# Kernel tuning notes

Hardware: AMD Instinct MI355X
Metric: run time of the kernel (lower is better)

Reference implementation:

```python
import jax, jax.numpy as jnp
import numpy as np

B = 128
N = 65536          # total nodes across batched subgraphs
E = 1048576        # total edges
CLIP_DIM = 768
PD = 512           # projection_dim


def setup_inputs() -> dict:
    key = jax.random.key(0)
    ks = jax.random.split(key, 20)
    s = 0.02
    return {
        # CLIP-encoded features (clip encoders treated as upstream feature extractors)
        "image_features": jax.random.normal(ks[0], (B, CLIP_DIM), jnp.float32),
        "text_features": jax.random.normal(ks[1], (B, CLIP_DIM), jnp.float32),
        "answer": jax.random.uniform(ks[2], (B,), jnp.float32),
        # batched subgraph (X_fixed rows already gathered, as in extract_subgraph_batch)
        "x_nodes": jax.random.normal(ks[3], (N, PD), jnp.float32),
        "edge_index": jax.random.randint(ks[4], (2, E), 0, N, jnp.int32),
        "batch_vec": jnp.sort(jax.random.randint(ks[5], (N,), 0, B, jnp.int32)),
        # image/text projections (clip_dim != projection_dim -> Linear)
        "W_img": jax.random.normal(ks[6], (CLIP_DIM, PD), jnp.float32) * s,
        "b_img": jnp.zeros((PD,), jnp.float32),
        "W_txt": jax.random.normal(ks[7], (CLIP_DIM, PD), jnp.float32) * s,
        "b_txt": jnp.zeros((PD,), jnp.float32),
        # implicit classifier: Linear(2*PD, PD) -> ReLU -> Linear(PD, 1)
        "W1": jax.random.normal(ks[8], (2 * PD, PD), jnp.float32) * s,
        "b1": jnp.zeros((PD,), jnp.float32),
        "W2": jax.random.normal(ks[9], (PD, 1), jnp.float32) * s,
        "b2": jnp.zeros((1,), jnp.float32),
        # GCNConv(PD, PD)
        "Wg": jax.random.normal(ks[10], (PD, PD), jnp.float32) * s,
        "bg": jnp.zeros((PD,), jnp.float32),
        # symbolic classifier: Linear(PD, PD) -> ReLU -> Linear(PD, 1)
        "Ws1": jax.random.normal(ks[11], (PD, PD), jnp.float32) * s,
        "bs1": jnp.zeros((PD,), jnp.float32),
        "Ws2": jax.random.normal(ks[12], (PD, 1), jnp.float32) * s,
        "bs2": jnp.zeros((1,), jnp.float32),
    }


def gcn_conv(x, edge_index, W, b):
    """PyG GCNConv: h = W x; add self-loops; sym-normalized sum aggregation."""
    n = x.shape[0]
    h = x @ W                                     # [N, PD] dense GEMM
    loop = jnp.arange(n, dtype=edge_index.dtype)
    src = jnp.concatenate([edge_index[0], loop])  # [E+N]
    dst = jnp.concatenate([edge_index[1], loop])
    deg = jax.ops.segment_sum(jnp.ones_like(dst, dtype=h.dtype), dst, num_segments=n)
    dis = jax.lax.rsqrt(deg)                      # deg >= 1 (self loops)
    norm = dis[src] * dis[dst]                    # [E+N]
    out = jax.ops.segment_sum(h[src] * norm[:, None], dst, num_segments=n)
    return out + b


def reference(image_features, text_features, answer, x_nodes, edge_index, batch_vec,
              W_img, b_img, W_txt, b_txt, W1, b1, W2, b2,
              Wg, bg, Ws1, bs1, Ws2, bs2):
    # ---- implicit branch (MedicalVQAModel.forward) ----
    img = image_features @ W_img + b_img          # [B, PD]
    txt = text_features @ W_txt + b_txt           # [B, PD]
    combined = jnp.concatenate([img, txt], axis=-1)
    h = jax.nn.relu(combined @ W1 + b1)           # dropout p=0.1 inactive (eval)
    y_implicit = (h @ W2 + b2)[:, 0]              # [B]

    # ---- symbolic branch: GCN over batched subgraphs ----
    x = gcn_conv(x_nodes, edge_index, Wg, bg)
    x = jax.nn.relu(x)                            # dropout p=0.8 inactive (eval)
    bv = batch_vec.astype(jnp.int32)
    sums = jax.ops.segment_sum(x, bv, num_segments=B)          # [B, PD]
    cnts = jax.ops.segment_sum(jnp.ones((x.shape[0],), x.dtype), bv, num_segments=B)
    graph_features = sums / jnp.maximum(cnts, 1.0)[:, None]    # global_mean_pool
    hs = jax.nn.relu(graph_features @ Ws1 + bs1)
    y_symbolic = (hs @ Ws2 + bs2)[:, 0]           # [B]

    logits = jnp.maximum(y_implicit, y_symbolic)
    # BCEWithLogits (mean): log(1+e^l) - l*y
    loss = jnp.mean(jnp.logaddexp(0.0, logits) - logits * answer)
    return (logits, loss)
```

## Files before the change

### kernel.cpp

```cpp
#include <hip/hip_runtime.h>
#include <stdint.h>

#define N_NODES 65536
#define N_EDGES 1048576
#define BATCH   128
#define PD      512
#define CLIPD   768

typedef __attribute__((ext_vector_type(4))) float f32x4;
typedef __attribute__((ext_vector_type(2))) float f32x2;
typedef __attribute__((ext_vector_type(4))) int   i32x4;

__device__ __forceinline__ unsigned short f2b(float f) {
    uint32_t u = __float_as_uint(f);
    return (unsigned short)((u + 0x7fffu + ((u >> 16) & 1u)) >> 16);
}

__global__ void k_wgt(const float* __restrict__ Wg, unsigned short* __restrict__ WgT,
                      const int* __restrict__ bv, int* __restrict__ cnts) {
    __shared__ float tile[32][33];
    int kb = blockIdx.x * 32, nb = blockIdx.y * 32;
    int tx = threadIdx.x, ty = threadIdx.y;
    if (kb == 0 && nb == 0) {
        int tid = ty * 32 + tx;
        if (tid < BATCH) {
            int lo = 0, hi = N_NODES;
            while (lo < hi) { int m = (lo + hi) >> 1; if (bv[m] < tid) lo = m + 1; else hi = m; }
            int lo2 = lo, hi2 = N_NODES;
            while (lo2 < hi2) { int m = (lo2 + hi2) >> 1; if (bv[m] < tid + 1) lo2 = m + 1; else hi2 = m; }
            cnts[tid] = lo2 - lo;
        }
    }
    tile[ty][tx] = Wg[(size_t)(kb + ty) * PD + nb + tx];
    __syncthreads();
    WgT[(size_t)(nb + ty) * PD + kb + tx] = f2b(tile[tx][ty]);
}

__global__ void k_init(int* __restrict__ deg, int* __restrict__ fill,
                       float* __restrict__ sums) {
    int i = blockIdx.x * 256 + threadIdx.x;
    deg[i] = 1;
    fill[i] = 0;
    sums[i] = 0.f;
}

__global__ void k_deg(const int* __restrict__ ei, int* __restrict__ deg) {
    int e = blockIdx.x * 256 + threadIdx.x;
    atomicAdd(&deg[ei[N_EDGES + e]], 1);
}

__global__ void k_scan(const int* __restrict__ deg, int* __restrict__ row_ptr,
                       float* __restrict__ dis) {
    __shared__ int wsum[16];
    const int t = threadIdx.x;
    const int w = t >> 6, l = t & 63;
    const int base = w * 4096;
    int s = 0;
    for (int i = 0; i < 64; ++i) s += deg[base + i * 64 + l];
    s -= 64;
#pragma unroll
    for (int off = 1; off < 64; off <<= 1) s += __shfl_xor(s, off);
    if (l == 0) wsum[w] = s;
    __syncthreads();
    int carry = 0;
    for (int i = 0; i < 16; ++i) carry += (i < w) ? wsum[i] : 0;
    int idx = base + l;
    int d = deg[idx];
    for (int i = 0; i < 64; ++i) {
        int dn = 0;
        if (i < 63) dn = deg[idx + 64];
        int v = d - 1;
        int inc = v;
#pragma unroll
        for (int off = 1; off < 64; off <<= 1) {
            int n = __shfl_up(inc, off);
            if (l >= off) inc += n;
        }
        row_ptr[idx] = carry + inc - v;
        dis[idx] = rsqrtf((float)d);
        carry += __shfl(inc, 63);
        idx += 64;
        d = dn;
    }
    if (t == 1023) row_ptr[N_NODES] = carry;
}

__global__ void k_scatter(const int* __restrict__ ei, const int* __restrict__ row_ptr,
                          int* __restrict__ fill, int* __restrict__ srcs) {
    int e = blockIdx.x * 256 + threadIdx.x;
    int d = ei[N_EDGES + e];
    int pos = row_ptr[d] + atomicAdd(&fill[d], 1);
    srcs[pos] = ei[e];
}

__device__ __forceinline__ void mfma16(f32x4& acc, i32x4 a, i32x4 b) {
    asm("v_mfma_f32_16x16x32_bf16 %0, %1, %2, %0" : "+v"(acc) : "v"(a), "v"(b));
}

__global__ __launch_bounds__(256) void k_gemm(const float* __restrict__ X,
                                              const unsigned short* __restrict__ WgT,
                                              const float* __restrict__ dis,
                                              uint8_t* __restrict__ hn8) {
    __shared__ __align__(16) unsigned short As[128 * 32];
    __shared__ __align__(16) unsigned short Bs[256 * 32];
    const int m0 = blockIdx.x * 128;
    const int n0 = blockIdx.y * 256;
    const int t = threadIdx.x;
    const int lane = t & 63, w = t >> 6;
    const int wr = w >> 1, wc = w & 1;
    const int g = lane >> 4, lr = lane & 15;

    f32x4 acc[4][8] = {};

    for (int k0 = 0; k0 < PD; k0 += 32) {
        __syncthreads();
#pragma unroll
        for (int it = 0; it < 4; ++it) {
            int idx = it * 256 + t;
            int r = idx >> 3, kc = (idx & 7) * 4;
            float4 v = *(const float4*)&X[(size_t)(m0 + r) * PD + k0 + kc];
            uint2 o;
            o.x = (uint32_t)f2b(v.x) | ((uint32_t)f2b(v.y) << 16);
            o.y = (uint32_t)f2b(v.z) | ((uint32_t)f2b(v.w) << 16);
            *(uint2*)&As[r * 32 + kc] = o;
        }
#pragma unroll
        for (int it = 0; it < 4; ++it) {
            int idx = it * 256 + t;
            int r = idx >> 2, kc = (idx & 3) * 8;
            *(uint4*)&Bs[r * 32 + kc] = *(const uint4*)&WgT[(size_t)(n0 + r) * PD + k0 + kc];
        }
        __syncthreads();

        i32x4 a[4], b[8];
#pragma unroll
        for (int i = 0; i < 4; ++i) a[i] = *(const i32x4*)&As[(wr * 64 + i * 16 + lr) * 32 + g * 8];
#pragma unroll
        for (int j = 0; j < 8; ++j) b[j] = *(const i32x4*)&Bs[(wc * 128 + j * 16 + lr) * 32 + g * 8];
#pragma unroll
        for (int i = 0; i < 4; ++i)
#pragma unroll
            for (int j = 0; j < 8; ++j) mfma16(acc[i][j], a[i], b[j]);
    }
    asm volatile("s_nop 7\n s_nop 7\n s_nop 7\n s_nop 7");

#pragma unroll
    for (int i = 0; i < 4; ++i) {
#pragma unroll
        for (int r = 0; r < 4; ++r) {
            int row = m0 + wr * 64 + i * 16 + g * 4 + r;
            float dd = dis[row];
#pragma unroll
            for (int j = 0; j < 8; ++j) {
                int col = n0 + wc * 128 + j * 16 + lr;
                float val = acc[i][j][r] * dd;
                uint32_t p = __builtin_amdgcn_cvt_pk_fp8_f32(val, val, 0, false);
                hn8[(size_t)row * PD + col] = (uint8_t)p;
            }
        }
    }
}

#define NPB 8
__global__ __launch_bounds__(256) void k_agg(const uint8_t* __restrict__ hn8,
                                             const float* __restrict__ dis,
                                             const float* __restrict__ bg,
                                             const int* __restrict__ row_ptr,
                                             const int* __restrict__ srcs,
                                             const int* __restrict__ bv,
                                             float* __restrict__ sums) {
    __shared__ __align__(16) float cmb[128 * 4];
    const int t = threadIdx.x;
    const int half = t >> 7, tl = t & 127;
    const int c0 = tl * 4;
    const int node0 = blockIdx.x * NPB;
    const float bg0 = bg[c0], bg1 = bg[c0 + 1], bg2 = bg[c0 + 2], bg3 = bg[c0 + 3];
    float s0 = 0.f, s1 = 0.f, s2 = 0.f, s3 = 0.f;
    int curb = bv[node0];
    for (int ni = 0; ni < NPB; ++ni) {
        int node = node0 + ni;
        int b = bv[node];
        if (b != curb) {
            if (half == 0) {
                atomicAdd(&sums[(size_t)curb * PD + c0 + 0], s0);
                atomicAdd(&sums[(size_t)curb * PD + c0 + 1], s1);
                atomicAdd(&sums[(size_t)curb * PD + c0 + 2], s2);
                atomicAdd(&sums[(size_t)curb * PD + c0 + 3], s3);
            }
            s0 = s1 = s2 = s3 = 0.f;
            curb = b;
        }
        float a0 = 0.f, a1 = 0.f, a2 = 0.f, a3 = 0.f;
        int beg = row_ptr[node], end = row_ptr[node + 1];
        int e = beg + half;
        for (; e + 14 < end; e += 16) {
            int sn[8];
#pragma unroll
            for (int q = 0; q < 8; ++q) sn[q] = srcs[e + 2 * q];
            uint32_t v[8];
#pragma unroll
            for (int q = 0; q < 8; ++q)
                v[q] = *(const uint32_t*)&hn8[(size_t)sn[q] * PD + c0];
#pragma unroll
            for (int q = 0; q < 8; ++q) {
                f32x2 lo = __builtin_amdgcn_cvt_pk_f32_fp8(v[q], false);
                f32x2 hi = __builtin_amdgcn_cvt_pk_f32_fp8(v[q], true);
                a0 += lo[0]; a1 += lo[1]; a2 += hi[0]; a3 += hi[1];
            }
        }
        for (; e < end; e += 2) {
            uint32_t v = *(const uint32_t*)&hn8[(size_t)srcs[e] * PD + c0];
            f32x2 lo = __builtin_amdgcn_cvt_pk_f32_fp8(v, false);
            f32x2 hi = __builtin_amdgcn_cvt_pk_f32_fp8(v, true);
            a0 += lo[0]; a1 += lo[1]; a2 += hi[0]; a3 += hi[1];
        }
        if (half == 1) {
            uint32_t v = *(const uint32_t*)&hn8[(size_t)node * PD + c0];
            f32x2 lo = __builtin_amdgcn_cvt_pk_f32_fp8(v, false);
            f32x2 hi = __builtin_amdgcn_cvt_pk_f32_fp8(v, true);
            a0 += lo[0]; a1 += lo[1]; a2 += hi[0]; a3 += hi[1];
            f32x4 wv = {a0, a1, a2, a3};
            *(f32x4*)&cmb[tl * 4] = wv;
        }
        __syncthreads();
        if (half == 0) {
            f32x4 ov = *(const f32x4*)&cmb[tl * 4];
            float dd = dis[node];
            a0 = fmaxf(fmaf(a0 + ov[0], dd, bg0), 0.f);
            a1 = fmaxf(fmaf(a1 + ov[1], dd, bg1), 0.f);
            a2 = fmaxf(fmaf(a2 + ov[2], dd, bg2), 0.f);
            a3 = fmaxf(fmaf(a3 + ov[3], dd, bg3), 0.f);
            s0 += a0; s1 += a1; s2 += a2; s3 += a3;
        }
        __syncthreads();
    }
    if (half == 0) {
        atomicAdd(&sums[(size_t)curb * PD + c0 + 0], s0);
        atomicAdd(&sums[(size_t)curb * PD + c0 + 1], s1);
        atomicAdd(&sums[(size_t)curb * PD + c0 + 2], s2);
        atomicAdd(&sums[(size_t)curb * PD + c0 + 3], s3);
    }
}

__device__ __forceinline__ void lin_part_core(const float* __restrict__ a,
                                              const float* __restrict__ wp,
                                              float* __restrict__ P, int slot, int c0) {
    float acc0 = 0.f, acc1 = 0.f, acc2 = 0.f, acc3 = 0.f;
    float acc4 = 0.f, acc5 = 0.f, acc6 = 0.f, acc7 = 0.f;
#pragma unroll 4
    for (int k = 0; k < 256; k += 8) {
        float a0 = a[k + 0], a1 = a[k + 1], a2 = a[k + 2], a3 = a[k + 3];
        float a4 = a[k + 4], a5 = a[k + 5], a6 = a[k + 6], a7 = a[k + 7];
        float2 w0 = *(const float2*)&wp[(size_t)(k + 0) * PD];
        float2 w1 = *(const float2*)&wp[(size_t)(k + 1) * PD];
        float2 w2 = *(const float2*)&wp[(size_t)(k + 2) * PD];
        float2 w3 = *(const float2*)&wp[(size_t)(k + 3) * PD];
        float2 w4 = *(const float2*)&wp[(size_t)(k + 4) * PD];
        float2 w5 = *(const float2*)&wp[(size_t)(k + 5) * PD];
        float2 w6 = *(const float2*)&wp[(size_t)(k + 6) * PD];
        float2 w7 = *(const float2*)&wp[(size_t)(k + 7) * PD];
        acc0 = fmaf(a0, w0.x, acc0); acc1 = fmaf(a0, w0.y, acc1);
        acc2 = fmaf(a1, w1.x, acc2); acc3 = fmaf(a1, w1.y, acc3);
        acc4 = fmaf(a2, w2.x, acc4); acc5 = fmaf(a2, w2.y, acc5);
        acc6 = fmaf(a3, w3.x, acc6); acc7 = fmaf(a3, w3.y, acc7);
        acc0 = fmaf(a4, w4.x, acc0); acc1 = fmaf(a4, w4.y, acc1);
        acc2 = fmaf(a5, w5.x, acc2); acc3 = fmaf(a5, w5.y, acc3);
        acc4 = fmaf(a6, w6.x, acc4); acc5 = fmaf(a6, w6.y, acc5);
        acc6 = fmaf(a7, w7.x, acc6); acc7 = fmaf(a7, w7.y, acc7);
    }
    P[(size_t)slot * PD + c0] = (acc0 + acc2) + (acc4 + acc6);
    P[(size_t)slot * PD + c0 + 1] = (acc1 + acc3) + (acc5 + acc7);
}

__global__ __launch_bounds__(256) void k_lin_part(const float* __restrict__ A,
                                                  const float* __restrict__ W,
                                                  float* __restrict__ P, int K) {
    const int row = blockIdx.x, kc = blockIdx.y, c0 = threadIdx.x * 2;
    lin_part_core(A + (size_t)row * K + kc * 256, W + (size_t)kc * 256 * PD + c0,
                  P, row * 8 + kc, c0);
}

__global__ __launch_bounds__(256) void k_lin_part_it(const float* __restrict__ IMG,
                                                     const float* __restrict__ TXT,
                                                     const float* __restrict__ Wi,
                                                     const float* __restrict__ Wt,
                                                     float* __restrict__ P) {
    const int row = blockIdx.x, kc = blockIdx.y, c0 = threadIdx.x * 2;
    const float* A = (kc < 3) ? IMG : TXT;
    const float* W = (kc < 3) ? Wi : Wt;
    const int sub = (kc < 3) ? kc : kc - 3;
    lin_part_core(A + (size_t)row * CLIPD + sub * 256, W + (size_t)sub * 256 * PD + c0,
                  P, row * 8 + kc, c0);
}

__global__ __launch_bounds__(256) void k_lin_red_it(const float* __restrict__ P,
                                                    const float* __restrict__ bi,
                                                    const float* __restrict__ bt,
                                                    float* __restrict__ C) {
    const int row = blockIdx.x, side = blockIdx.y, c0 = threadIdx.x * 2;
    const float* p = P + ((size_t)row * 8 + side * 3) * PD + c0;
    float r0 = p[0] + p[PD] + p[2 * PD];
    float r1 = p[1] + p[PD + 1] + p[2 * PD + 1];
    const float* bias = side ? bt : bi;
    C[(size_t)row * 1024 + side * PD + c0] = r0 + bias[c0];
    C[(size_t)row * 1024 + side * PD + c0 + 1] = r1 + bias[c0 + 1];
}

__global__ __launch_bounds__(256) void k_reddot(const float* __restrict__ P,
                                                const float* __restrict__ bias,
                                                const float* __restrict__ w2,
                                                const float* __restrict__ b2,
                                                float* __restrict__ y,
                                                int nch, const int* __restrict__ cnts) {
    __shared__ float wred[4];
    const int row = blockIdx.x;
    const int t = threadIdx.x;
    const int c0 = t * 2;
    const float* p = P + (size_t)row * 8 * PD + c0;
    float r0 = p[0], r1 = p[1];
    if (nch > 1) { r0 += p[PD];     r1 += p[PD + 1]; }
    if (nch > 2) { r0 += p[2 * PD]; r1 += p[2 * PD + 1]; }
    if (nch > 3) { r0 += p[3 * PD]; r1 += p[3 * PD + 1]; }
    float s = 1.f;
    if (cnts) s = 1.f / fmaxf((float)cnts[row], 1.f);
    r0 = fmaxf(fmaf(r0, s, bias[c0]), 0.f);
    r1 = fmaxf(fmaf(r1, s, bias[c0 + 1]), 0.f);
    float partial = fmaf(r0, w2[c0], r1 * w2[c0 + 1]);
#pragma unroll
    for (int off = 32; off; off >>= 1) partial += __shfl_down(partial, off);
    if ((t & 63) == 0) wred[t >> 6] = partial;
    __syncthreads();
    if (t == 0) y[row] = (wred[0] + wred[1]) + (wred[2] + wred[3]) + b2[0];
}

__global__ void k_final(const float* __restrict__ yi, const float* __restrict__ ys,
                        const float* __restrict__ ans, float* __restrict__ out) {
    __shared__ float red[128];
    int t = threadIdx.x;
    float l = fmaxf(yi[t], ys[t]);
    out[t] = l;
    float li = fmaxf(l, 0.f) + log1pf(expf(-fabsf(l))) - l * ans[t];
    red[t] = li;
    __syncthreads();
    for (int off = 64; off; off >>= 1) {
        if (t < off) red[t] += red[t + off];
        __syncthreads();
    }
    if (t == 0) out[BATCH] = red[0] / (float)BATCH;
}

extern "C" void kernel_launch(void* const* d_in, const int* in_sizes, int n_in,
                              void* d_out, int out_size, void* d_ws, size_t ws_size,
                              hipStream_t stream) {
    const float* image_features = (const float*)d_in[0];
    const float* text_features  = (const float*)d_in[1];
    const float* answer         = (const float*)d_in[2];
    const float* x_nodes        = (const float*)d_in[3];
    const int*   edge_index     = (const int*)d_in[4];
    const int*   batch_vec      = (const int*)d_in[5];
    const float* W_img = (const float*)d_in[6];
    const float* b_img = (const float*)d_in[7];
    const float* W_txt = (const float*)d_in[8];
    const float* b_txt = (const float*)d_in[9];
    const float* W1  = (const float*)d_in[10];
    const float* b1  = (const float*)d_in[11];
    const float* W2  = (const float*)d_in[12];
    const float* b2  = (const float*)d_in[13];
    const float* Wg  = (const float*)d_in[14];
    const float* bg  = (const float*)d_in[15];
    const float* Ws1 = (const float*)d_in[16];
    const float* bs1 = (const float*)d_in[17];
    const float* Ws2 = (const float*)d_in[18];
    const float* bs2 = (const float*)d_in[19];
    float* out = (float*)d_out;

    char* base = (char*)d_ws;
    size_t cur = 0;
    auto alloc = [&](size_t bytes) -> void* {
        void* r = base + cur;
        cur = (cur + bytes + 255) & ~(size_t)255;
        return r;
    };
    unsigned short* WgT = (unsigned short*)alloc((size_t)PD * PD * 2);
    uint8_t* hn8   = (uint8_t*)alloc((size_t)N_NODES * PD);
    int*   deg     = (int*)alloc((size_t)N_NODES * 4);
    float* dis     = (float*)alloc((size_t)N_NODES * 4);
    int*   row_ptr = (int*)alloc((size_t)(N_NODES + 1) * 4);
    int*   fill    = (int*)alloc((size_t)N_NODES * 4);
    int*   srcs    = (int*)alloc((size_t)N_EDGES * 4);
    float* sums    = (float*)alloc((size_t)BATCH * PD * 4);
    int*   cnts    = (int*)alloc((size_t)BATCH * 4);
    float* Ppart   = (float*)alloc((size_t)BATCH * 8 * PD * 4);
    float* combined = (float*)alloc((size_t)BATCH * 1024 * 4);
    float* yi      = (float*)alloc((size_t)BATCH * 4);
    float* ys      = (float*)alloc((size_t)BATCH * 4);

    hipLaunchKernelGGL(k_wgt, dim3(16, 16), dim3(32, 32), 0, stream, Wg, WgT, batch_vec, cnts);
    hipLaunchKernelGGL(k_init, dim3(256), dim3(256), 0, stream, deg, fill, sums);
    hipLaunchKernelGGL(k_deg, dim3(4096), dim3(256), 0, stream, edge_index, deg);
    hipLaunchKernelGGL(k_scan, dim3(1), dim3(1024), 0, stream, deg, row_ptr, dis);
    hipLaunchKernelGGL(k_scatter, dim3(4096), dim3(256), 0, stream, edge_index, row_ptr, fill, srcs);
    hipLaunchKernelGGL(k_gemm, dim3(N_NODES / 128, PD / 256), dim3(256), 0, stream,
                       x_nodes, WgT, dis, hn8);
    hipLaunchKernelGGL(k_agg, dim3(N_NODES / NPB), dim3(256), 0, stream,
                       hn8, dis, bg, row_ptr, srcs, batch_vec, sums);

    hipLaunchKernelGGL(k_lin_part_it, dim3(BATCH, 6), dim3(256), 0, stream,
                       image_features, text_features, W_img, W_txt, Ppart);
    hipLaunchKernelGGL(k_lin_red_it, dim3(BATCH, 2), dim3(256), 0, stream,
                       Ppart, b_img, b_txt, combined);
    hipLaunchKernelGGL(k_lin_part, dim3(BATCH, 4), dim3(256), 0, stream,
                       combined, W1, Ppart, 1024);
    hipLaunchKernelGGL(k_reddot, dim3(BATCH), dim3(256), 0, stream,
                       Ppart, b1, W2, b2, yi, 4, (const int*)nullptr);

    hipLaunchKernelGGL(k_lin_part, dim3(BATCH, 2), dim3(256), 0, stream,
                       sums, Ws1, Ppart, PD);
    hipLaunchKernelGGL(k_reddot, dim3(BATCH), dim3(256), 0, stream,
                       Ppart, bs1, Ws2, bs2, ys, 2, cnts);

    hipLaunchKernelGGL(k_final, dim3(1), dim3(128), 0, stream, yi, ys, answer, out);
}
```

Baseline: 411.8 us.

## Assign one wavefront per node run in GCN aggregation, drop block syncs

The aggregation kernel changes from a 256-thread block splitting each node's edges across two halves, which were combined through shared memory with two __syncthreads per node, to each 64-lane wavefront handling its own run of 8 nodes. Each lane now covers 8 channels with 8-byte fp8 loads. This removes the shared-memory combine and block barriers and widens per-lane gathers. In exchange each node's edges are walked serially by one wave, so per-node latency grows, and there are four times as many atomic streams into the pooled sums.

```diff
diff --git a/kernel.cpp b/kernel.cpp
--- a/kernel.cpp
+++ b/kernel.cpp
@@ -161,7 +161,16 @@
     }
 }
 
-#define NPB 8
+#define NPW 8
+__device__ __forceinline__ void acc8(float a[8], uint2 v) {
+    f32x2 l0 = __builtin_amdgcn_cvt_pk_f32_fp8(v.x, false);
+    f32x2 h0 = __builtin_amdgcn_cvt_pk_f32_fp8(v.x, true);
+    f32x2 l1 = __builtin_amdgcn_cvt_pk_f32_fp8(v.y, false);
+    f32x2 h1 = __builtin_amdgcn_cvt_pk_f32_fp8(v.y, true);
+    a[0] += l0[0]; a[1] += l0[1]; a[2] += h0[0]; a[3] += h0[1];
+    a[4] += l1[0]; a[5] += l1[1]; a[6] += h1[0]; a[7] += h1[1];
+}
+
 __global__ __launch_bounds__(256) void k_agg(const uint8_t* __restrict__ hn8,
                                              const float* __restrict__ dis,
                                              const float* __restrict__ bg,
@@ -169,77 +178,56 @@
                                              const int* __restrict__ srcs,
                                              const int* __restrict__ bv,
                                              float* __restrict__ sums) {
-    __shared__ __align__(16) float cmb[128 * 4];
     const int t = threadIdx.x;
-    const int half = t >> 7, tl = t & 127;
-    const int c0 = tl * 4;
-    const int node0 = blockIdx.x * NPB;
-    const float bg0 = bg[c0], bg1 = bg[c0 + 1], bg2 = bg[c0 + 2], bg3 = bg[c0 + 3];
-    float s0 = 0.f, s1 = 0.f, s2 = 0.f, s3 = 0.f;
+    const int w = t >> 6, lane = t & 63;
+    const int c0 = lane * 8;
+    const int node0 = (blockIdx.x * 4 + w) * NPW;
+    float bgv[8];
+#pragma unroll
+    for (int j = 0; j < 8; ++j) bgv[j] = bg[c0 + j];
+    float s[8] = {};
     int curb = bv[node0];
-    for (int ni = 0; ni < NPB; ++ni) {
+    for (int ni = 0; ni < NPW; ++ni) {
         int node = node0 + ni;
         int b = bv[node];
         if (b != curb) {
-            if (half == 0) {
-                atomicAdd(&sums[(size_t)curb * PD + c0 + 0], s0);
-                atomicAdd(&sums[(size_t)curb * PD + c0 + 1], s1);
-                atomicAdd(&sums[(size_t)curb * PD + c0 + 2], s2);
-                atomicAdd(&sums[(size_t)curb * PD + c0 + 3], s3);
-            }
-            s0 = s1 = s2 = s3 = 0.f;
+#pragma unroll
+            for (int j = 0; j < 8; ++j) atomicAdd(&sums[(size_t)curb * PD + c0 + j], s[j]);
+#pragma unroll
+            for (int j = 0; j < 8; ++j) s[j] = 0.f;
             curb = b;
         }
-        float a0 = 0.f, a1 = 0.f, a2 = 0.f, a3 = 0.f;
+        float a[8] = {};
         int beg = row_ptr[node], end = row_ptr[node + 1];
-        int e = beg + half;
-        for (; e + 14 < end; e += 16) {
+        int e = beg;
+        for (; e + 8 <= end; e += 8) {
             int sn[8];
 #pragma unroll
-            for (int q = 0; q < 8; ++q) sn[q] = srcs[e + 2 * q];
-            uint32_t v[8];
+            for (int q = 0; q < 8; ++q) sn[q] = srcs[e + q];
+            uint2 v[8];
 #pragma unroll
             for (int q = 0; q < 8; ++q)
-                v[q] = *(const uint32_t*)&hn8[(size_t)sn[q] * PD + c0];
-#pragma unroll
-            for (int q = 0; q < 8; ++q) {
-                f32x2 lo = __builtin_amdgcn_cvt_pk_f32_fp8(v[q], false);
-                f32x2 hi = __builtin_amdgcn_cvt_pk_f32_fp8(v[q], true);
-                a0 += lo[0]; a1 += lo[1]; a2 += hi[0]; a3 += hi[1];
-            }
-        }
-        for (; e < end; e += 2) {
-            uint32_t v = *(const uint32_t*)&hn8[(size_t)srcs[e] * PD + c0];
-            f32x2 lo = __builtin_amdgcn_cvt_pk_f32_fp8(v, false);
-            f32x2 hi = __builtin_amdgcn_cvt_pk_f32_fp8(v, true);
-            a0 += lo[0]; a1 += lo[1]; a2 += hi[0]; a3 += hi[1];
-        }
-        if (half == 1) {
-            uint32_t v = *(const uint32_t*)&hn8[(size_t)node * PD + c0];
-            f32x2 lo = __builtin_amdgcn_cvt_pk_f32_fp8(v, false);
-            f32x2 hi = __builtin_amdgcn_cvt_pk_f32_fp8(v, true);
-            a0 += lo[0]; a1 += lo[1]; a2 += hi[0]; a3 += hi[1];
-            f32x4 wv = {a0, a1, a2, a3};
-            *(f32x4*)&cmb[tl * 4] = wv;
-        }
-        __syncthreads();
-        if (half == 0) {
-            f32x4 ov = *(const f32x4*)&cmb[tl * 4];
-            float dd = dis[node];
-            a0 = fmaxf(fmaf(a0 + ov[0], dd, bg0), 0.f);
-            a1 = fmaxf(fmaf(a1 + ov[1], dd, bg1), 0.f);
-            a2 = fmaxf(fmaf(a2 + ov[2], dd, bg2), 0.f);
-            a3 = fmaxf(fmaf(a3 + ov[3], dd, bg3), 0.f);
-            s0 += a0; s1 += a1; s2 += a2; s3 += a3;
-        }
-        __syncthreads();
-    }
-    if (half == 0) {
-        atomicAdd(&sums[(size_t)curb * PD + c0 + 0], s0);
-        atomicAdd(&sums[(size_t)curb * PD + c0 + 1], s1);
-        atomicAdd(&sums[(size_t)curb * PD + c0 + 2], s2);
-        atomicAdd(&sums[(size_t)curb * PD + c0 + 3], s3);
-    }
+                v[q] = *(const uint2*)&hn8[(size_t)sn[q] * PD + c0];
+#pragma unroll
+            for (int q = 0; q < 8; ++q) acc8(a, v[q]);
+        }
+        for (; e < end; ++e) {
+            uint2 v = *(const uint2*)&hn8[(size_t)srcs[e] * PD + c0];
+            acc8(a, v);
+        }
+        {
+            uint2 v = *(const uint2*)&hn8[(size_t)node * PD + c0];
+            acc8(a, v);
+        }
+        float dd = dis[node];
+#pragma unroll
+        for (int j = 0; j < 8; ++j) {
+            float r = fmaxf(fmaf(a[j], dd, bgv[j]), 0.f);
+            s[j] += r;
+        }
+    }
+#pragma unroll
+    for (int j = 0; j < 8; ++j) atomicAdd(&sums[(size_t)curb * PD + c0 + j], s[j]);
 }
 
 __device__ __forceinline__ void lin_part_core(const float* __restrict__ a,
@@ -402,7 +390,7 @@
     hipLaunchKernelGGL(k_scatter, dim3(4096), dim3(256), 0, stream, edge_index, row_ptr, fill, srcs);
     hipLaunchKernelGGL(k_gemm, dim3(N_NODES / 128, PD / 256), dim3(256), 0, stream,
                        x_nodes, WgT, dis, hn8);
-    hipLaunchKernelGGL(k_agg, dim3(N_NODES / NPB), dim3(256), 0, stream,
+    hipLaunchKernelGGL(k_agg, dim3(N_NODES / (NPW * 4)), dim3(256), 0, stream,
                        hn8, dis, bg, row_ptr, srcs, batch_vec, sums);
 
     hipLaunchKernelGGL(k_lin_part_it, dim3(BATCH, 6), dim3(256), 0, stream,
```

After: 442.0 us. +7.3%, slower.
